# Kernel tuning notes

Hardware: AMD Instinct MI355X
Metric: run time of the kernel (lower is better)

The kernel has to match this reference:

```python
import jax, jax.numpy as jnp
import numpy as np
import math

C = 768          # in_channels
KC = 768         # key_channels
VC = 768         # value_channels
H = 12           # head_count
B, N = 8, 2048


def setup_inputs() -> dict:
    key = jax.random.key(0)
    ks = jax.random.split(key, 9)
    s = 0.02
    return {
        "x": jax.random.normal(ks[0], (B, N, C), dtype=jnp.float32),
        # Linear weights stored as (in, out); y = x @ W + b
        "Wq": jax.random.normal(ks[1], (C, KC), dtype=jnp.float32) * s,
        "bq": jnp.zeros((KC,), dtype=jnp.float32),
        "Wk": jax.random.normal(ks[2], (C, KC), dtype=jnp.float32) * s,
        "bk": jnp.zeros((KC,), dtype=jnp.float32),
        "Wv": jax.random.normal(ks[3], (C, VC), dtype=jnp.float32) * s,
        "bv": jnp.zeros((VC,), dtype=jnp.float32),
        "Wr": jax.random.normal(ks[4], (VC, C), dtype=jnp.float32) * s,
        "br": jnp.zeros((C,), dtype=jnp.float32),
    }


def reference(x, Wq, bq, Wk, bk, Wv, bv, Wr, br):
    b, n, c = x.shape
    dk = KC // H  # head key channels
    dv = VC // H  # head value channels
    q = (x @ Wq + bq).reshape(b, n, H, dk)
    k = (x @ Wk + bk).reshape(b, n, H, dk)
    v = (x @ Wv + bv).reshape(b, n, H, dv)
    # NOTE: original scales by sqrt(N) (sequence length), not sqrt(d_head)
    scores = jnp.einsum("bqhd,bkhd->bhqk", q, k) / math.sqrt(n)
    attn = jax.nn.softmax(scores, axis=-1)
    out = jnp.einsum("bhqk,bkhd->bqhd", attn, v).reshape(b, n, VC)
    # reprojection + relu; dropout is identity in eval mode
    return jax.nn.relu(out @ Wr + br)
```

## Files before the change

### kernel.cpp

```cpp
#include <hip/hip_runtime.h>
#include <math.h>

typedef unsigned short u16;
typedef short short8 __attribute__((ext_vector_type(8)));
typedef float f32x4 __attribute__((ext_vector_type(4)));

#define BATCH 8
#define SEQ   2048
#define CH    768
#define NH    12
#define DH    64
#define BH    (BATCH*NH)
#define MTOT  (BATCH*SEQ)

#if __has_builtin(__builtin_amdgcn_exp2f)
#define EXP2F(x) __builtin_amdgcn_exp2f(x)
#else
#define EXP2F(x) exp2f(x)
#endif

#define GL2L(g, l) __builtin_amdgcn_global_load_lds( \
    (const __attribute__((address_space(1))) void*)(g), \
    (__attribute__((address_space(3))) void*)(l), 16, 0, 0)

#define BARRIER_LDS()  asm volatile("s_waitcnt lgkmcnt(0)\n\ts_barrier" ::: "memory")
#define BARRIER_FULL() asm volatile("s_waitcnt vmcnt(0) lgkmcnt(0)\n\ts_barrier" ::: "memory")

__device__ __forceinline__ float bf2f(u16 u) {
  union { unsigned int i; float f; } v; v.i = ((unsigned int)u) << 16; return v.f;
}
__device__ __forceinline__ u16 f2bf(float f) {
  union { float f; unsigned int i; } v; v.f = f;
  return (u16)((v.i + 0x7fffu + ((v.i >> 16) & 1u)) >> 16);
}
__device__ __forceinline__ u16 f2bf_rtz(float f) {
  union { float f; unsigned int i; } v; v.f = f;
  return (u16)(v.i >> 16);
}

__global__ void sniff_k(const u16* __restrict__ x, int* __restrict__ flag) {
  __shared__ int cnt;
  if (threadIdx.x == 0) cnt = 0;
  __syncthreads();
  int big = 0;
  for (int i = 0; i < 8; ++i) {
    u16 u = x[threadIdx.x + i * 256];
    int e = (u >> 7) & 0xFF;
    if (e >= 0x89) big++;
  }
  atomicAdd(&cnt, big);
  __syncthreads();
  if (threadIdx.x == 0) *flag = (cnt > 4) ? 1 : 0;
}

__global__ __launch_bounds__(256) void cvt_x_k(const void* __restrict__ xin,
                                               u16* __restrict__ xb,
                                               const int* __restrict__ flag) {
  int i4 = (blockIdx.x * 256 + threadIdx.x) * 4;
  if (*flag) {
    float4 f = *(const float4*)((const float*)xin + i4);
    ushort4 o;
    o.x = f2bf(f.x); o.y = f2bf(f.y); o.z = f2bf(f.z); o.w = f2bf(f.w);
    *(ushort4*)(xb + i4) = o;
  } else {
    *(ushort4*)(xb + i4) = *(const ushort4*)((const u16*)xin + i4);
  }
}

__global__ void cvt_bias_k(const void* b0, const void* b1, const void* b2, const void* b3,
                           u16* __restrict__ biasb, const int* __restrict__ flag) {
  int isf = *flag;
  for (int t = threadIdx.x; t < 4 * CH; t += 256) {
    int wz = t / CH, c = t - wz * CH;
    const void* src = (wz == 0) ? b0 : (wz == 1) ? b1 : (wz == 2) ? b2 : b3;
    biasb[t] = isf ? f2bf(((const float*)src)[c]) : ((const u16*)src)[c];
  }
}

__global__ __launch_bounds__(256) void transpose_w4_k(u16* __restrict__ wt,
    const void* w0, const void* w1, const void* w2, const void* w3,
    const int* __restrict__ flag) {
  __shared__ __align__(16) u16 t[64][65];
  const int z = blockIdx.z;
  const void* in = (z == 0) ? w0 : (z == 1) ? w1 : (z == 2) ? w2 : w3;
  u16* out = wt + (size_t)z * CH * CH;
  const int tid = threadIdx.x;
  const int r0 = blockIdx.y * 64, c0 = blockIdx.x * 64;
  const int isf = *flag;
#pragma unroll
  for (int i = 0; i < 16; ++i) {
    int idx = i * 256 + tid;
    int row = idx >> 6, col = idx & 63;
    size_t g = (size_t)(r0 + row) * CH + c0 + col;
    t[row][col] = isf ? f2bf(((const float*)in)[g]) : ((const u16*)in)[g];
  }
  __syncthreads();
#pragma unroll
  for (int i = 0; i < 16; ++i) {
    int idx = i * 256 + tid;
    int orow = idx >> 6, ocol = idx & 63;
    out[(size_t)(c0 + orow) * CH + r0 + ocol] = t[ocol][orow];
  }
}

template <int EPI>
__global__ __launch_bounds__(256) void gemm_bt_k(
    const u16* __restrict__ A, const u16* __restrict__ BtBase,
    const u16* __restrict__ biasb, u16* __restrict__ outBase,
    u16* __restrict__ voutBase, void* __restrict__ finalOut,
    const int* __restrict__ flag, float qscale) {
  const int K = CH;
  const int tid = threadIdx.x;
  const int wv = tid >> 6, lane = tid & 63, quad = lane >> 4, l16 = lane & 15;
  const int wm = (wv >> 1) * 64, wn = (wv & 1) * 64;

  const int id = blockIdx.x;
  const int xcd = id & 7, u = id >> 3;
  int n0, m0, z;
  if (EPI == 0) {
    int n0z = u % 18, yl = u / 18;
    n0 = (n0z % 6) * 128; z = n0z / 6;
    m0 = (xcd + 8 * yl) * 128;
  } else {
    int n0z = u % 6, yl = u / 6;
    n0 = n0z * 128; z = 3;
    m0 = (xcd + 8 * yl) * 128;
  }
  const u16* Bt = BtBase + (size_t)z * CH * CH;
  const u16* bias = biasb + (size_t)z * CH;

  __shared__ __align__(16) u16 As[128 * 64];
  __shared__ __align__(16) u16 Bs[128 * 64];

  const f32x4 fz4 = {0.f, 0.f, 0.f, 0.f};
  f32x4 acc[4][4];
#pragma unroll
  for (int mt = 0; mt < 4; ++mt)
#pragma unroll
    for (int nt = 0; nt < 4; ++nt) acc[mt][nt] = fz4;

  for (int kt = 0; kt < K; kt += 64) {
#pragma unroll
    for (int i = 0; i < 4; ++i) {
      int c = tid + i * 256;
      int r = c >> 3;
      int pg = (c & 7) ^ (r & 7);
      GL2L(A + (size_t)(m0 + r) * K + kt + pg * 8, As + c * 8);
    }
#pragma unroll
    for (int i = 0; i < 4; ++i) {
      int c = tid + i * 256;
      int r = c >> 3;
      int pg = (c & 7) ^ (r & 7);
      GL2L(Bt + (size_t)(n0 + r) * K + kt + pg * 8, Bs + c * 8);
    }
    __syncthreads();

    short8 af[4][2], bf[4][2];
#pragma unroll
    for (int mt = 0; mt < 4; ++mt) {
      int r = wm + mt * 16 + l16;
#pragma unroll
      for (int ks = 0; ks < 2; ++ks) {
        int p = (ks * 4 + quad) ^ (r & 7);
        af[mt][ks] = *(const short8*)(As + r * 64 + p * 8);
      }
    }
#pragma unroll
    for (int nt = 0; nt < 4; ++nt) {
      int r = wn + nt * 16 + l16;
#pragma unroll
      for (int ks = 0; ks < 2; ++ks) {
        int p = (ks * 4 + quad) ^ (r & 7);
        bf[nt][ks] = *(const short8*)(Bs + r * 64 + p * 8);
      }
    }
#pragma unroll
    for (int ks = 0; ks < 2; ++ks)
#pragma unroll
      for (int mt = 0; mt < 4; ++mt)
#pragma unroll
        for (int nt = 0; nt < 4; ++nt)
          acc[mt][nt] = __builtin_amdgcn_mfma_f32_16x16x32_bf16(af[mt][ks], bf[nt][ks],
                                                                acc[mt][nt], 0, 0, 0);
    __syncthreads();
  }

  const int of32 = (EPI == 1) ? *flag : 0;
#pragma unroll
  for (int mt = 0; mt < 4; ++mt) {
#pragma unroll
    for (int nt = 0; nt < 4; ++nt) {
      int col = n0 + wn + nt * 16 + l16;
      float bv = bf2f(bias[col]);
      int rowb = m0 + wm + mt * 16 + quad * 4;
      if (EPI == 1) {
#pragma unroll
        for (int r = 0; r < 4; ++r) {
          float vv = fmaxf(acc[mt][nt][r] + bv, 0.0f);
          size_t off = (size_t)(rowb + r) * CH + col;
          if (of32) ((float*)finalOut)[off] = vv;
          else      ((u16*)finalOut)[off] = f2bf(vv);
        }
      } else if (z == 2) {
        int b = rowb >> 11, n = rowb & (SEQ - 1);
        int h = col >> 6, d = col & 63;
        ushort4 pk;
        pk.x = f2bf(acc[mt][nt][0] + bv);
        pk.y = f2bf(acc[mt][nt][1] + bv);
        pk.z = f2bf(acc[mt][nt][2] + bv);
        pk.w = f2bf(acc[mt][nt][3] + bv);
        *(ushort4*)(voutBase + ((size_t)((b * NH + h) * DH + d)) * SEQ + n) = pk;
      } else {
        float sc = (z == 0) ? qscale : 1.0f;
#pragma unroll
        for (int r = 0; r < 4; ++r) {
          float vv = (acc[mt][nt][r] + bv) * sc;
          int row = rowb + r;
          int b = row >> 11, n = row & (SEQ - 1);
          int h = col >> 6, d = col & 63;
          outBase[(size_t)z * BH * SEQ * DH + ((size_t)(b * NH + h) * SEQ + n) * DH + d] = f2bf(vv);
        }
      }
    }
  }
}

__global__ __launch_bounds__(256, 3) void flash_attn_k(
    const u16* __restrict__ Qg, const u16* __restrict__ Kg,
    const u16* __restrict__ Vtg, u16* __restrict__ Og) {
  const int tid = threadIdx.x;
  const int wv = tid >> 6, lane = tid & 63, quad = lane >> 4, l16 = lane & 15;
  const int id = blockIdx.x;
  const int bh = (id & 7) + 8 * (id >> 7);
  const int q0 = ((id >> 3) & 15) * 128;
  const int b = bh / NH, h = bh - b * NH;

  __shared__ __align__(16) u16 smem[24576];
  u16* Ps = smem + 16384;

  const f32x4 fz4 = {0.f, 0.f, 0.f, 0.f};

  const u16* Qp = Qg + (size_t)bh * SEQ * DH + (size_t)q0 * DH;
  const u16* Kp = Kg + (size_t)bh * SEQ * DH;
  const u16* Vp = Vtg + (size_t)bh * DH * SEQ;

#pragma unroll
  for (int i = 0; i < 4; ++i) {
    int c = tid + i * 256; int r = c >> 3; int pg = (c & 7) ^ (r & 7);
    GL2L(Qp + (size_t)r * DH + pg * 8, Ps + c * 8);
  }
#pragma unroll
  for (int i = 0; i < 2; ++i) {
    int c = tid + i * 256; int r = c >> 3; int pg = (c & 7) ^ (r & 7);
    GL2L(Kp + (size_t)r * DH + pg * 8, smem + c * 8);
    GL2L(Vp + (size_t)r * SEQ + pg * 8, smem + 4096 + c * 8);
  }
  __syncthreads();

  short8 qf[2][2];
#pragma unroll
  for (int mt = 0; mt < 2; ++mt) {
    int r = wv * 32 + mt * 16 + l16;
#pragma unroll
    for (int ks = 0; ks < 2; ++ks) {
      int p = (ks * 4 + quad) ^ (r & 7);
      qf[mt][ks] = *(const short8*)(Ps + r * 64 + p * 8);
    }
  }

  float lsum[2][4];
  f32x4 oacc[2][4];
#pragma unroll
  for (int mt = 0; mt < 2; ++mt)
#pragma unroll
    for (int r = 0; r < 4; ++r) lsum[mt][r] = 0.f;
#pragma unroll
  for (int mt = 0; mt < 2; ++mt)
#pragma unroll
    for (int dt = 0; dt < 4; ++dt) oacc[mt][dt] = fz4;

  int cur = 0;
  for (int k0 = 0; k0 < SEQ; k0 += 64) {
    BARRIER_FULL();
    u16* Ks = smem + cur * 8192;
    u16* Vs = Ks + 4096;
    if (k0 + 64 < SEQ) {
      int k1 = k0 + 64;
      u16* Kn = smem + (cur ^ 1) * 8192;
#pragma unroll
      for (int i = 0; i < 2; ++i) {
        int c = tid + i * 256; int r = c >> 3; int pg = (c & 7) ^ (r & 7);
        GL2L(Kp + (size_t)(k1 + r) * DH + pg * 8, Kn + c * 8);
        GL2L(Vp + (size_t)r * SEQ + k1 + pg * 8, Kn + 4096 + c * 8);
      }
    }

    f32x4 s[2][4];
#pragma unroll
    for (int mt = 0; mt < 2; ++mt)
#pragma unroll
      for (int nt = 0; nt < 4; ++nt) s[mt][nt] = fz4;
#pragma unroll
    for (int nt = 0; nt < 4; ++nt) {
      int r = nt * 16 + l16;
#pragma unroll
      for (int ks = 0; ks < 2; ++ks) {
        int p = (ks * 4 + quad) ^ (r & 7);
        short8 kf = *(const short8*)(Ks + r * 64 + p * 8);
        s[0][nt] = __builtin_amdgcn_mfma_f32_16x16x32_bf16(qf[0][ks], kf, s[0][nt], 0, 0, 0);
        s[1][nt] = __builtin_amdgcn_mfma_f32_16x16x32_bf16(qf[1][ks], kf, s[1][nt], 0, 0, 0);
      }
    }

#pragma unroll
    for (int mt = 0; mt < 2; ++mt)
#pragma unroll
      for (int nt = 0; nt < 4; ++nt) {
        int colc = nt * 16 + l16;
        int ch = colc >> 3, off8 = colc & 7;
#pragma unroll
        for (int r = 0; r < 4; ++r) {
          float p = EXP2F(s[mt][nt][r]);
          lsum[mt][r] += p;
          int row = wv * 32 + mt * 16 + quad * 4 + r;
          Ps[row * 64 + ((ch ^ (row & 7)) * 8) + off8] = f2bf_rtz(p);
        }
      }
    BARRIER_LDS();

#pragma unroll
    for (int ks = 0; ks < 2; ++ks) {
      short8 pf[2];
#pragma unroll
      for (int mt = 0; mt < 2; ++mt) {
        int r = wv * 32 + mt * 16 + l16;
        int p = (ks * 4 + quad) ^ (r & 7);
        pf[mt] = *(const short8*)(Ps + r * 64 + p * 8);
      }
#pragma unroll
      for (int dt = 0; dt < 4; ++dt) {
        int rv = dt * 16 + l16;
        int p = (ks * 4 + quad) ^ (rv & 7);
        short8 vf = *(const short8*)(Vs + rv * 64 + p * 8);
        oacc[0][dt] = __builtin_amdgcn_mfma_f32_16x16x32_bf16(pf[0], vf, oacc[0][dt], 0, 0, 0);
        oacc[1][dt] = __builtin_amdgcn_mfma_f32_16x16x32_bf16(pf[1], vf, oacc[1][dt], 0, 0, 0);
      }
    }
    cur ^= 1;
  }

#pragma unroll
  for (int mt = 0; mt < 2; ++mt)
#pragma unroll
    for (int r = 0; r < 4; ++r) {
      float v = lsum[mt][r];
#pragma unroll
      for (int off = 1; off < 16; off <<= 1) v += __shfl_xor(v, off, 64);
      lsum[mt][r] = 1.0f / v;
    }

#pragma unroll
  for (int mt = 0; mt < 2; ++mt)
#pragma unroll
    for (int r = 0; r < 4; ++r) {
      float inv = lsum[mt][r];
      int qi = q0 + wv * 32 + mt * 16 + quad * 4 + r;
      size_t base = ((size_t)(b * SEQ) + qi) * CH + h * DH;
#pragma unroll
      for (int dt = 0; dt < 4; ++dt) {
        int d = dt * 16 + l16;
        Og[base + d] = f2bf(oacc[mt][dt][r] * inv);
      }
    }
}

extern "C" void kernel_launch(void* const* d_in, const int* in_sizes, int n_in,
                              void* d_out, int out_size, void* d_ws, size_t ws_size,
                              hipStream_t stream) {
  const void* x  = d_in[0];
  const void* Wq = d_in[1];
  const void* bq = d_in[2];
  const void* Wk = d_in[3];
  const void* bk = d_in[4];
  const void* Wv = d_in[5];
  const void* bv = d_in[6];
  const void* Wr = d_in[7];
  const void* br = d_in[8];
  u16* ws = (u16*)d_ws;

  const size_t WSZ = (size_t)CH * CH;
  const size_t XSZ = (size_t)MTOT * CH;
  int* flag  = (int*)ws;
  u16* biasb = ws + 8;
  u16* wt    = ws + 4096;
  u16* xb    = wt + 4 * WSZ;
  u16* q     = xb + XSZ;
  u16* k     = q + XSZ;
  u16* vt    = k + XSZ;

  const float qscale = (float)(1.4426950408889634 / sqrt(2048.0));

  sniff_k<<<1, 256, 0, stream>>>((const u16*)x, flag);
  cvt_x_k<<<XSZ / 1024, 256, 0, stream>>>(x, xb, flag);
  cvt_bias_k<<<1, 256, 0, stream>>>(bq, bk, bv, br, biasb, flag);
  transpose_w4_k<<<dim3(12, 12, 4), 256, 0, stream>>>(wt, Wq, Wk, Wv, Wr, flag);
  gemm_bt_k<0><<<dim3(2304), 256, 0, stream>>>(xb, wt, biasb, q, vt, nullptr,
                                               flag, qscale);
  u16* ao = xb;
  flash_attn_k<<<dim3(1536), 256, 0, stream>>>(q, k, vt, ao);
  gemm_bt_k<1><<<dim3(768), 256, 0, stream>>>(ao, wt, biasb, nullptr, nullptr,
                                              d_out, flag, 1.0f);
}
```

Baseline: 379.7 us.

## Transpose QK^T MFMA so each lane owns a query row and packs P writes

Swaps the MFMA operand order so the score accumulator holds four consecutive key columns for a single query row per lane. This lets each lane pack four bf16 probabilities into one 8-byte LDS store instead of four scalar stores, and turns the row-sum reduction into two cross-quad shuffles. It also drops the LDS barrier between the P write and the P@V read, relying on each wave touching only its own rows, with a compiler memory fence in its place. The risk is an LDS hazard if the rows are not really wave-private, plus an extra shuffle in the epilogue to hand the inverse sums back to the output layout.

```diff
diff --git a/kernel.cpp b/kernel.cpp
--- a/kernel.cpp
+++ b/kernel.cpp
@@ -23,7 +23,6 @@
     (const __attribute__((address_space(1))) void*)(g), \
     (__attribute__((address_space(3))) void*)(l), 16, 0, 0)
 
-#define BARRIER_LDS()  asm volatile("s_waitcnt lgkmcnt(0)\n\ts_barrier" ::: "memory")
 #define BARRIER_FULL() asm volatile("s_waitcnt vmcnt(0) lgkmcnt(0)\n\ts_barrier" ::: "memory")
 
 __device__ __forceinline__ float bf2f(u16 u) {
@@ -32,10 +31,6 @@
 __device__ __forceinline__ u16 f2bf(float f) {
   union { float f; unsigned int i; } v; v.f = f;
   return (u16)((v.i + 0x7fffu + ((v.i >> 16) & 1u)) >> 16);
-}
-__device__ __forceinline__ u16 f2bf_rtz(float f) {
-  union { float f; unsigned int i; } v; v.f = f;
-  return (u16)(v.i >> 16);
 }
 
 __global__ void sniff_k(const u16* __restrict__ x, int* __restrict__ flag) {
@@ -269,12 +264,8 @@
     }
   }
 
-  float lsum[2][4];
+  float lsum[2] = {0.f, 0.f};
   f32x4 oacc[2][4];
-#pragma unroll
-  for (int mt = 0; mt < 2; ++mt)
-#pragma unroll
-    for (int r = 0; r < 4; ++r) lsum[mt][r] = 0.f;
 #pragma unroll
   for (int mt = 0; mt < 2; ++mt)
 #pragma unroll
@@ -308,26 +299,31 @@
       for (int ks = 0; ks < 2; ++ks) {
         int p = (ks * 4 + quad) ^ (r & 7);
         short8 kf = *(const short8*)(Ks + r * 64 + p * 8);
-        s[0][nt] = __builtin_amdgcn_mfma_f32_16x16x32_bf16(qf[0][ks], kf, s[0][nt], 0, 0, 0);
-        s[1][nt] = __builtin_amdgcn_mfma_f32_16x16x32_bf16(qf[1][ks], kf, s[1][nt], 0, 0, 0);
-      }
-    }
-
-#pragma unroll
-    for (int mt = 0; mt < 2; ++mt)
+        s[0][nt] = __builtin_amdgcn_mfma_f32_16x16x32_bf16(kf, qf[0][ks], s[0][nt], 0, 0, 0);
+        s[1][nt] = __builtin_amdgcn_mfma_f32_16x16x32_bf16(kf, qf[1][ks], s[1][nt], 0, 0, 0);
+      }
+    }
+
+#pragma unroll
+    for (int mt = 0; mt < 2; ++mt) {
+      int row = wv * 32 + mt * 16 + l16;
+      u16* prow = Ps + row * 64 + (quad & 1) * 4;
+      int sw = row & 7;
 #pragma unroll
       for (int nt = 0; nt < 4; ++nt) {
-        int colc = nt * 16 + l16;
-        int ch = colc >> 3, off8 = colc & 7;
-#pragma unroll
-        for (int r = 0; r < 4; ++r) {
-          float p = EXP2F(s[mt][nt][r]);
-          lsum[mt][r] += p;
-          int row = wv * 32 + mt * 16 + quad * 4 + r;
-          Ps[row * 64 + ((ch ^ (row & 7)) * 8) + off8] = f2bf_rtz(p);
-        }
-      }
-    BARRIER_LDS();
+        float p0 = EXP2F(s[mt][nt][0]);
+        float p1 = EXP2F(s[mt][nt][1]);
+        float p2 = EXP2F(s[mt][nt][2]);
+        float p3 = EXP2F(s[mt][nt][3]);
+        lsum[mt] += (p0 + p1) + (p2 + p3);
+        uint2 w;
+        w.x = __builtin_amdgcn_perm(__float_as_uint(p1), __float_as_uint(p0), 0x07060302u);
+        w.y = __builtin_amdgcn_perm(__float_as_uint(p3), __float_as_uint(p2), 0x07060302u);
+        int c16 = (nt * 2 + (quad >> 1)) ^ sw;
+        *(uint2*)(prow + c16 * 8) = w;
+      }
+    }
+    asm volatile("" ::: "memory");
 
 #pragma unroll
     for (int ks = 0; ks < 2; ++ks) {
@@ -351,20 +347,18 @@
   }
 
 #pragma unroll
+  for (int mt = 0; mt < 2; ++mt) {
+    float v = lsum[mt];
+    v += __shfl_xor(v, 16, 64);
+    v += __shfl_xor(v, 32, 64);
+    lsum[mt] = 1.0f / v;
+  }
+
+#pragma unroll
   for (int mt = 0; mt < 2; ++mt)
 #pragma unroll
     for (int r = 0; r < 4; ++r) {
-      float v = lsum[mt][r];
-#pragma unroll
-      for (int off = 1; off < 16; off <<= 1) v += __shfl_xor(v, off, 64);
-      lsum[mt][r] = 1.0f / v;
-    }
-
-#pragma unroll
-  for (int mt = 0; mt < 2; ++mt)
-#pragma unroll
-    for (int r = 0; r < 4; ++r) {
-      float inv = lsum[mt][r];
+      float inv = __shfl(lsum[mt], quad * 4 + r, 16);
       int qi = q0 + wv * 32 + mt * 16 + quad * 4 + r;
       size_t base = ((size_t)(b * SEQ) + qi) * CH + h * DH;
 #pragma unroll
```

Measured after the change: 371.6 us. 1.02x faster.
